# Optimization experiments

Measured on AMD Instinct MI355X. Metric: run time of the kernel, lower is better.

Reference implementation:

```python
import jax, jax.numpy as jnp
import numpy as np

NEG_BIG = -9e15
ALPHA = 0.2  # LeakyReLU negative slope


def setup_inputs() -> dict:
    key = jax.random.key(0)
    k1, k2, k3, k4 = jax.random.split(key, 4)
    B, N, Fin, Fout = 4, 2048, 128, 128
    h = jax.random.normal(k1, (B, N, Fin), dtype=jnp.float32)
    adj = jax.random.randint(k2, (N, N), 0, 2, dtype=jnp.int32)
    W = jax.random.normal(k3, (Fin, Fout), dtype=jnp.float32) * 0.1
    a = jax.random.normal(k4, (2 * Fout, 1), dtype=jnp.float32) * 0.1
    return {"h": h, "adj": adj, "W": W, "a": a}


def reference(h, adj, W, a):
    # Wh: [B, N, Fout]
    Wh = jnp.einsum('bnf,fo->bno', h, W)
    Fout = W.shape[1]
    a1 = a[:Fout, 0]   # attends to source i
    a2 = a[Fout:, 0]   # attends to target j
    # Decomposed form of leakyrelu(cat([Wh_i, Wh_j]) @ a):
    # e_ij = leakyrelu(a1.Wh_i + a2.Wh_j)  -> [B, N, N]
    f1 = Wh @ a1  # [B, N]
    f2 = Wh @ a2  # [B, N]
    e = jax.nn.leaky_relu(f1[:, :, None] + f2[:, None, :], negative_slope=ALPHA)
    attention = jnp.where(adj[None, :, :] > 0, e, jnp.float32(NEG_BIG))
    attention = jax.nn.softmax(attention, axis=2)
    # dropout is identity in eval mode
    h_prime = jnp.einsum('bij,bjo->bio', attention, Wh)
    return h_prime
```

## Files before the change

### kernel.cpp

```cpp
#include <hip/hip_runtime.h>

#define BB 4
#define NN 2048
#define FF 128
#define NP 2176
#define ALPHA 0.2f
#define SHIFT_C 16.0f

typedef short bf16x8 __attribute__((ext_vector_type(8)));
typedef float f32x4 __attribute__((ext_vector_type(4)));
typedef unsigned u32;

__device__ inline short f2bf(float f) {
    union { float f; unsigned u; } v; v.f = f;
    unsigned r = (v.u + 0x7FFFu + ((v.u >> 16) & 1u)) >> 16;
    return (short)r;
}
__device__ inline float bf2f(short s) {
    union { float f; unsigned u; } v;
    v.u = ((unsigned)(unsigned short)s) << 16;
    return v.f;
}

__global__ __launch_bounds__(256) void k_wh(const float* __restrict__ h,
                                            const float* __restrict__ W,
                                            const float* __restrict__ a,
                                            const int* __restrict__ adj,
                                            short* __restrict__ WhHiT,
                                            short* __restrict__ WhLoT,
                                            float* __restrict__ f1,
                                            float* __restrict__ f2,
                                            u32* __restrict__ adjp) {
    __shared__ float Wa[2 * FF];
    __shared__ float hs[16 * 128];
    int tid = threadIdx.x;
    int r0 = blockIdx.x * 16;

    {
        int fin = tid & 127;
        const float* av = (tid < 128) ? a : (a + FF);
        const float* wr = W + (size_t)fin * FF;
        float s = 0.f;
        for (int o = 0; o < FF; o += 4) {
            float4 wv = *(const float4*)(wr + o);
            float4 avv = *(const float4*)(av + o);
            s += wv.x * avv.x + wv.y * avv.y + wv.z * avv.z + wv.w * avv.w;
        }
        Wa[(tid < 128 ? 0 : FF) + fin] = s;
    }
    {
        const float4* src = (const float4*)(h + (size_t)r0 * FF);
        float4* dst = (float4*)hs;
        dst[tid] = src[tid];
        dst[256 + tid] = src[256 + tid];
    }
    {
        int g = blockIdx.x * 256 + tid;
        int row = g >> 6, wd = g & 63;
        const int4* ar = (const int4*)(adj + (size_t)row * NN + wd * 32);
        u32 word = 0;
#pragma unroll
        for (int q = 0; q < 8; ++q) {
            int4 v = ar[q];
            word |= (u32)(v.x > 0) << (q * 4);
            word |= (u32)(v.y > 0) << (q * 4 + 1);
            word |= (u32)(v.z > 0) << (q * 4 + 2);
            word |= (u32)(v.w > 0) << (q * 4 + 3);
        }
        adjp[row * 64 + wd] = word;
    }
    __syncthreads();

    {
        int w = tid >> 6, lane = tid & 63;
        float wa1_0 = Wa[lane], wa1_1 = Wa[lane + 64];
        float wa2_0 = Wa[FF + lane], wa2_1 = Wa[FF + lane + 64];
        for (int rr = 0; rr < 4; ++rr) {
            int rloc = w * 4 + rr;
            int row = r0 + rloc;
            float x0 = hs[rloc * FF + lane], x1 = hs[rloc * FF + lane + 64];
            float s1 = x0 * wa1_0 + x1 * wa1_1;
            float s2 = x0 * wa2_0 + x1 * wa2_1;
#pragma unroll
            for (int m = 32; m >= 1; m >>= 1) {
                s1 += __shfl_xor(s1, m, 64);
                s2 += __shfl_xor(s2, m, 64);
            }
            if (lane == 0) { f1[row] = s1; f2[row] = s2; }
        }
    }

    int f4 = (tid & 31) * 4;
    int rg = tid >> 5;
    float acc[2][4];
#pragma unroll
    for (int rr = 0; rr < 2; ++rr)
#pragma unroll
        for (int cc = 0; cc < 4; ++cc) acc[rr][cc] = 0.f;

    for (int k0 = 0; k0 < FF; k0 += 4) {
        float4 wv[4];
#pragma unroll
        for (int kk = 0; kk < 4; ++kk)
            wv[kk] = *(const float4*)(W + (size_t)(k0 + kk) * FF + f4);
        float4 hv[2];
#pragma unroll
        for (int rr = 0; rr < 2; ++rr)
            hv[rr] = *(const float4*)(hs + (rg * 2 + rr) * FF + k0);
#pragma unroll
        for (int rr = 0; rr < 2; ++rr) {
            float hk[4] = {hv[rr].x, hv[rr].y, hv[rr].z, hv[rr].w};
#pragma unroll
            for (int kk = 0; kk < 4; ++kk) {
                acc[rr][0] += hk[kk] * wv[kk].x;
                acc[rr][1] += hk[kk] * wv[kk].y;
                acc[rr][2] += hk[kk] * wv[kk].z;
                acc[rr][3] += hk[kk] * wv[kk].w;
            }
        }
    }
    int rloc = r0 + rg * 2;
    int b = rloc >> 11;
    int j = rloc & (NN - 1);
#pragma unroll
    for (int cc = 0; cc < 4; ++cc) {
        float v0 = acc[0][cc], v1 = acc[1][cc];
        short h0 = f2bf(v0), h1 = f2bf(v1);
        short l0 = f2bf(v0 - bf2f(h0)), l1 = f2bf(v1 - bf2f(h1));
        size_t off = (size_t)(b * FF + f4 + cc) * NP + j;
        *(short2*)(WhHiT + off) = make_short2(h0, h1);
        *(short2*)(WhLoT + off) = make_short2(l0, l1);
    }
}

#define EV(f2v, f1v, wv, bi) ({ float _t = (f1v) + (f2v); float _x = fmaxf(_t, ALPHA * _t); \
    __expf(_x - SHIFT_C) * (float)(((wv) >> (bi)) & 1u); })

__global__ __launch_bounds__(512) __attribute__((amdgpu_waves_per_eu(4, 4)))
void k_attn(const short* __restrict__ WhHiT,
            const short* __restrict__ WhLoT,
            const u32* __restrict__ adjp,
            const float* __restrict__ f1,
            const float* __restrict__ f2,
            float* __restrict__ out) {
    __shared__ __align__(16) char lds[66688];
    float* row_ps = (float*)(lds + 65536);
    float* row_inv = (float*)(lds + 66560);

    int tid = threadIdx.x;
    int w = tid >> 6, lane = tid & 63;
    int blk = blockIdx.x;
    int b = blk >> 7;
    int tile = (blk >> 1) & 63;
    int half = blk & 1;
    int i0 = tile * 32;

    int r_c = lane & 15, kg = lane >> 4;

    const float* f2b = f2 + b * NN;
    float f10 = f1[b * NN + i0 + r_c];
    float f11 = f1[b * NN + i0 + 16 + r_c];
    const u32* ap0 = adjp + (size_t)(i0 + r_c) * 64;
    const u32* ap1 = adjp + (size_t)(i0 + 16 + r_c) * 64;

    const ptrdiff_t dLo = (ptrdiff_t)BB * FF * NP;
    int s0 = w * 8;
    const short* pB0 = WhHiT + (size_t)(b * FF + half * 64 + 0 * 16 + r_c) * NP + s0 * 32 + kg * 8;
    const short* pB1 = WhHiT + (size_t)(b * FF + half * 64 + 1 * 16 + r_c) * NP + s0 * 32 + kg * 8;
    const short* pB2 = WhHiT + (size_t)(b * FF + half * 64 + 2 * 16 + r_c) * NP + s0 * 32 + kg * 8;
    const short* pB3 = WhHiT + (size_t)(b * FF + half * 64 + 3 * 16 + r_c) * NP + s0 * 32 + kg * 8;

    f32x4 acc0_0 = {0,0,0,0}, acc0_1 = {0,0,0,0};
    f32x4 acc1_0 = {0,0,0,0}, acc1_1 = {0,0,0,0};
    f32x4 acc2_0 = {0,0,0,0}, acc2_1 = {0,0,0,0};
    f32x4 acc3_0 = {0,0,0,0}, acc3_1 = {0,0,0,0};
    float sp0 = 0.f, sp1 = 0.f;

#pragma unroll 1
    for (int s8 = 0; s8 < 8; ++s8) {
        int s = s0 + s8;
        float4 q0 = *(const float4*)(f2b + s * 32 + kg * 8);
        float4 q1 = *(const float4*)(f2b + s * 32 + kg * 8 + 4);
        u32 w0 = ap0[s], w1 = ap1[s];
        bf16x8 bh0 = *(const bf16x8*)(pB0); bf16x8 bl0 = *(const bf16x8*)(pB0 + dLo);
        bf16x8 bh1 = *(const bf16x8*)(pB1); bf16x8 bl1 = *(const bf16x8*)(pB1 + dLo);
        bf16x8 bh2 = *(const bf16x8*)(pB2); bf16x8 bl2 = *(const bf16x8*)(pB2 + dLo);
        bf16x8 bh3 = *(const bf16x8*)(pB3); bf16x8 bl3 = *(const bf16x8*)(pB3 + dLo);

        union { u32 u[4]; bf16x8 v; } A0, A1;
        int bb = kg * 8;
        {
            float pa, pb;
            pa = EV(q0.x, f10, w0, bb + 0); pb = EV(q0.y, f10, w0, bb + 1);
            sp0 += pa + pb;
            asm("v_cvt_pk_bf16_f32 %0, %1, %2" : "=v"(A0.u[0]) : "v"(pa), "v"(pb));
            pa = EV(q0.z, f10, w0, bb + 2); pb = EV(q0.w, f10, w0, bb + 3);
            sp0 += pa + pb;
            asm("v_cvt_pk_bf16_f32 %0, %1, %2" : "=v"(A0.u[1]) : "v"(pa), "v"(pb));
            pa = EV(q1.x, f10, w0, bb + 4); pb = EV(q1.y, f10, w0, bb + 5);
            sp0 += pa + pb;
            asm("v_cvt_pk_bf16_f32 %0, %1, %2" : "=v"(A0.u[2]) : "v"(pa), "v"(pb));
            pa = EV(q1.z, f10, w0, bb + 6); pb = EV(q1.w, f10, w0, bb + 7);
            sp0 += pa + pb;
            asm("v_cvt_pk_bf16_f32 %0, %1, %2" : "=v"(A0.u[3]) : "v"(pa), "v"(pb));

            pa = EV(q0.x, f11, w1, bb + 0); pb = EV(q0.y, f11, w1, bb + 1);
            sp1 += pa + pb;
            asm("v_cvt_pk_bf16_f32 %0, %1, %2" : "=v"(A1.u[0]) : "v"(pa), "v"(pb));
            pa = EV(q0.z, f11, w1, bb + 2); pb = EV(q0.w, f11, w1, bb + 3);
            sp1 += pa + pb;
            asm("v_cvt_pk_bf16_f32 %0, %1, %2" : "=v"(A1.u[1]) : "v"(pa), "v"(pb));
            pa = EV(q1.x, f11, w1, bb + 4); pb = EV(q1.y, f11, w1, bb + 5);
            sp1 += pa + pb;
            asm("v_cvt_pk_bf16_f32 %0, %1, %2" : "=v"(A1.u[2]) : "v"(pa), "v"(pb));
            pa = EV(q1.z, f11, w1, bb + 6); pb = EV(q1.w, f11, w1, bb + 7);
            sp1 += pa + pb;
            asm("v_cvt_pk_bf16_f32 %0, %1, %2" : "=v"(A1.u[3]) : "v"(pa), "v"(pb));
        }

        acc0_0 = __builtin_amdgcn_mfma_f32_16x16x32_bf16(A0.v, bh0, acc0_0, 0, 0, 0);
        acc0_0 = __builtin_amdgcn_mfma_f32_16x16x32_bf16(A0.v, bl0, acc0_0, 0, 0, 0);
        acc0_1 = __builtin_amdgcn_mfma_f32_16x16x32_bf16(A1.v, bh0, acc0_1, 0, 0, 0);
        acc0_1 = __builtin_amdgcn_mfma_f32_16x16x32_bf16(A1.v, bl0, acc0_1, 0, 0, 0);
        acc1_0 = __builtin_amdgcn_mfma_f32_16x16x32_bf16(A0.v, bh1, acc1_0, 0, 0, 0);
        acc1_0 = __builtin_amdgcn_mfma_f32_16x16x32_bf16(A0.v, bl1, acc1_0, 0, 0, 0);
        acc1_1 = __builtin_amdgcn_mfma_f32_16x16x32_bf16(A1.v, bh1, acc1_1, 0, 0, 0);
        acc1_1 = __builtin_amdgcn_mfma_f32_16x16x32_bf16(A1.v, bl1, acc1_1, 0, 0, 0);
        acc2_0 = __builtin_amdgcn_mfma_f32_16x16x32_bf16(A0.v, bh2, acc2_0, 0, 0, 0);
        acc2_0 = __builtin_amdgcn_mfma_f32_16x16x32_bf16(A0.v, bl2, acc2_0, 0, 0, 0);
        acc2_1 = __builtin_amdgcn_mfma_f32_16x16x32_bf16(A1.v, bh2, acc2_1, 0, 0, 0);
        acc2_1 = __builtin_amdgcn_mfma_f32_16x16x32_bf16(A1.v, bl2, acc2_1, 0, 0, 0);
        acc3_0 = __builtin_amdgcn_mfma_f32_16x16x32_bf16(A0.v, bh3, acc3_0, 0, 0, 0);
        acc3_0 = __builtin_amdgcn_mfma_f32_16x16x32_bf16(A0.v, bl3, acc3_0, 0, 0, 0);
        acc3_1 = __builtin_amdgcn_mfma_f32_16x16x32_bf16(A1.v, bh3, acc3_1, 0, 0, 0);
        acc3_1 = __builtin_amdgcn_mfma_f32_16x16x32_bf16(A1.v, bl3, acc3_1, 0, 0, 0);

        pB0 += 32; pB1 += 32; pB2 += 32; pB3 += 32;
    }

    sp0 += __shfl_xor(sp0, 16, 64); sp0 += __shfl_xor(sp0, 32, 64);
    sp1 += __shfl_xor(sp1, 16, 64); sp1 += __shfl_xor(sp1, 32, 64);
    if (lane < 16) {
        row_ps[w * 32 + lane] = sp0;
        row_ps[w * 32 + 16 + lane] = sp1;
    }
    {
        char* img = lds + w * 8192;
#define STACC(NI, MI, A) { int ch = (((NI)*16 + r_c) * 8 + (MI)*4 + kg) ^ (r_c & 7); \
                           *(f32x4*)(img + ch * 16) = (A); }
        STACC(0, 0, acc0_0) STACC(0, 1, acc0_1)
        STACC(1, 0, acc1_0) STACC(1, 1, acc1_1)
        STACC(2, 0, acc2_0) STACC(2, 1, acc2_1)
        STACC(3, 0, acc3_0) STACC(3, 1, acc3_1)
#undef STACC
    }
    __syncthreads();
    if (tid < 32) {
        float t = 0.f;
#pragma unroll
        for (int ww = 0; ww < 8; ++ww) t += row_ps[ww * 32 + tid];
        row_inv[tid] = 1.0f / t;
    }
    __syncthreads();

    {
        int colg = w * 8 + (lane >> 3);
        int rq = lane & 7;
        int ch = (colg * 8 + rq) ^ (colg & 7);
        f32x4 v = {0, 0, 0, 0};
#pragma unroll
        for (int im = 0; im < 8; ++im)
            v += *(const f32x4*)(lds + im * 8192 + ch * 16);
        f32x4 rinv = *(const f32x4*)((char*)row_inv + rq * 16);
        float* ob = out + ((size_t)b * NN + i0 + rq * 4) * FF + half * 64 + colg;
#pragma unroll
        for (int q = 0; q < 4; ++q)
            ob[(size_t)q * FF] = v[q] * rinv[q];
    }
}

extern "C" void kernel_launch(void* const* d_in, const int* in_sizes, int n_in,
                              void* d_out, int out_size, void* d_ws, size_t ws_size,
                              hipStream_t stream) {
    const float* h   = (const float*)d_in[0];
    const int*   adj = (const int*)d_in[1];
    const float* W   = (const float*)d_in[2];
    const float* a   = (const float*)d_in[3];
    float* out = (float*)d_out;

    short* WhHiT = (short*)d_ws;
    short* WhLoT = WhHiT + (size_t)BB * FF * NP;
    float* f1 = (float*)(WhLoT + (size_t)BB * FF * NP);
    float* f2 = f1 + (size_t)BB * NN;
    u32* adjp = (u32*)(f2 + (size_t)BB * NN);

    k_wh<<<(BB * NN) / 16, 256, 0, stream>>>(h, W, a, adj, WhHiT, WhLoT, f1, f2, adjp);
    k_attn<<<512, 512, 0, stream>>>(WhHiT, WhLoT, adjp, f1, f2, out);
}
```

Before: 133.2 us.

## Split attention output columns into quarters to double grid and shrink LDS

Each k_attn block now computes 32 output features instead of 64, so the grid grows from 512 to 1024 blocks and per-thread accumulators halve. The cross-wave reduction uses half the LDS: waves 0-3 store partials, waves 4-7 add theirs in place, and the final pass sums 4 images instead of 8. This is meant to raise occupancy and parallelism on the 256-CU part. In exchange, the exp/softmax score computation and the f2/adjacency loads are duplicated across four blocks instead of two.

Result: slower. 241.5 us (+81.3%).

```diff
diff --git a/kernel.cpp b/kernel.cpp
--- a/kernel.cpp
+++ b/kernel.cpp
@@ -136,23 +136,23 @@
 #define EV(f2v, f1v, wv, bi) ({ float _t = (f1v) + (f2v); float _x = fmaxf(_t, ALPHA * _t); \
     __expf(_x - SHIFT_C) * (float)(((wv) >> (bi)) & 1u); })
 
-__global__ __launch_bounds__(512) __attribute__((amdgpu_waves_per_eu(4, 4)))
+__global__ __launch_bounds__(512, 8)
 void k_attn(const short* __restrict__ WhHiT,
             const short* __restrict__ WhLoT,
             const u32* __restrict__ adjp,
             const float* __restrict__ f1,
             const float* __restrict__ f2,
             float* __restrict__ out) {
-    __shared__ __align__(16) char lds[66688];
-    float* row_ps = (float*)(lds + 65536);
-    float* row_inv = (float*)(lds + 66560);
+    __shared__ __align__(16) char lds[17536];
+    float* row_ps = (float*)(lds + 16384);
+    float* row_inv = (float*)(lds + 17408);
 
     int tid = threadIdx.x;
     int w = tid >> 6, lane = tid & 63;
     int blk = blockIdx.x;
-    int b = blk >> 7;
-    int tile = (blk >> 1) & 63;
-    int half = blk & 1;
+    int b = blk >> 8;
+    int tile = (blk >> 2) & 63;
+    int qt = blk & 3;
     int i0 = tile * 32;
 
     int r_c = lane & 15, kg = lane >> 4;
@@ -165,15 +165,11 @@
 
     const ptrdiff_t dLo = (ptrdiff_t)BB * FF * NP;
     int s0 = w * 8;
-    const short* pB0 = WhHiT + (size_t)(b * FF + half * 64 + 0 * 16 + r_c) * NP + s0 * 32 + kg * 8;
-    const short* pB1 = WhHiT + (size_t)(b * FF + half * 64 + 1 * 16 + r_c) * NP + s0 * 32 + kg * 8;
-    const short* pB2 = WhHiT + (size_t)(b * FF + half * 64 + 2 * 16 + r_c) * NP + s0 * 32 + kg * 8;
-    const short* pB3 = WhHiT + (size_t)(b * FF + half * 64 + 3 * 16 + r_c) * NP + s0 * 32 + kg * 8;
+    const short* pB0 = WhHiT + (size_t)(b * FF + qt * 32 + 0 * 16 + r_c) * NP + s0 * 32 + kg * 8;
+    const short* pB1 = WhHiT + (size_t)(b * FF + qt * 32 + 1 * 16 + r_c) * NP + s0 * 32 + kg * 8;
 
     f32x4 acc0_0 = {0,0,0,0}, acc0_1 = {0,0,0,0};
     f32x4 acc1_0 = {0,0,0,0}, acc1_1 = {0,0,0,0};
-    f32x4 acc2_0 = {0,0,0,0}, acc2_1 = {0,0,0,0};
-    f32x4 acc3_0 = {0,0,0,0}, acc3_1 = {0,0,0,0};
     float sp0 = 0.f, sp1 = 0.f;
 
 #pragma unroll 1
@@ -184,8 +180,6 @@
         u32 w0 = ap0[s], w1 = ap1[s];
         bf16x8 bh0 = *(const bf16x8*)(pB0); bf16x8 bl0 = *(const bf16x8*)(pB0 + dLo);
         bf16x8 bh1 = *(const bf16x8*)(pB1); bf16x8 bl1 = *(const bf16x8*)(pB1 + dLo);
-        bf16x8 bh2 = *(const bf16x8*)(pB2); bf16x8 bl2 = *(const bf16x8*)(pB2 + dLo);
-        bf16x8 bh3 = *(const bf16x8*)(pB3); bf16x8 bl3 = *(const bf16x8*)(pB3 + dLo);
 
         union { u32 u[4]; bf16x8 v; } A0, A1;
         int bb = kg * 8;
@@ -226,16 +220,8 @@
         acc1_0 = __builtin_amdgcn_mfma_f32_16x16x32_bf16(A0.v, bl1, acc1_0, 0, 0, 0);
         acc1_1 = __builtin_amdgcn_mfma_f32_16x16x32_bf16(A1.v, bh1, acc1_1, 0, 0, 0);
         acc1_1 = __builtin_amdgcn_mfma_f32_16x16x32_bf16(A1.v, bl1, acc1_1, 0, 0, 0);
-        acc2_0 = __builtin_amdgcn_mfma_f32_16x16x32_bf16(A0.v, bh2, acc2_0, 0, 0, 0);
-        acc2_0 = __builtin_amdgcn_mfma_f32_16x16x32_bf16(A0.v, bl2, acc2_0, 0, 0, 0);
-        acc2_1 = __builtin_amdgcn_mfma_f32_16x16x32_bf16(A1.v, bh2, acc2_1, 0, 0, 0);
-        acc2_1 = __builtin_amdgcn_mfma_f32_16x16x32_bf16(A1.v, bl2, acc2_1, 0, 0, 0);
-        acc3_0 = __builtin_amdgcn_mfma_f32_16x16x32_bf16(A0.v, bh3, acc3_0, 0, 0, 0);
-        acc3_0 = __builtin_amdgcn_mfma_f32_16x16x32_bf16(A0.v, bl3, acc3_0, 0, 0, 0);
-        acc3_1 = __builtin_amdgcn_mfma_f32_16x16x32_bf16(A1.v, bh3, acc3_1, 0, 0, 0);
-        acc3_1 = __builtin_amdgcn_mfma_f32_16x16x32_bf16(A1.v, bl3, acc3_1, 0, 0, 0);
-
-        pB0 += 32; pB1 += 32; pB2 += 32; pB3 += 32;
+
+        pB0 += 32; pB1 += 32;
     }
 
     sp0 += __shfl_xor(sp0, 16, 64); sp0 += __shfl_xor(sp0, 32, 64);
@@ -244,18 +230,23 @@
         row_ps[w * 32 + lane] = sp0;
         row_ps[w * 32 + 16 + lane] = sp1;
     }
-    {
-        char* img = lds + w * 8192;
+    if (w < 4) {
+        char* img = lds + w * 4096;
 #define STACC(NI, MI, A) { int ch = (((NI)*16 + r_c) * 8 + (MI)*4 + kg) ^ (r_c & 7); \
                            *(f32x4*)(img + ch * 16) = (A); }
         STACC(0, 0, acc0_0) STACC(0, 1, acc0_1)
         STACC(1, 0, acc1_0) STACC(1, 1, acc1_1)
-        STACC(2, 0, acc2_0) STACC(2, 1, acc2_1)
-        STACC(3, 0, acc3_0) STACC(3, 1, acc3_1)
 #undef STACC
     }
     __syncthreads();
-    if (tid < 32) {
+    if (w >= 4) {
+        char* img = lds + (w - 4) * 4096;
+#define MRGACC(NI, MI, A) { int ch = (((NI)*16 + r_c) * 8 + (MI)*4 + kg) ^ (r_c & 7); \
+                            f32x4* p = (f32x4*)(img + ch * 16); *p = *p + (A); }
+        MRGACC(0, 0, acc0_0) MRGACC(0, 1, acc0_1)
+        MRGACC(1, 0, acc1_0) MRGACC(1, 1, acc1_1)
+#undef MRGACC
+    } else if (tid < 32) {
         float t = 0.f;
 #pragma unroll
         for (int ww = 0; ww < 8; ++ww) t += row_ps[ww * 32 + tid];
@@ -263,16 +254,16 @@
     }
     __syncthreads();
 
-    {
-        int colg = w * 8 + (lane >> 3);
+    if (lane < 32) {
+        int colg = w * 4 + (lane >> 3);
         int rq = lane & 7;
         int ch = (colg * 8 + rq) ^ (colg & 7);
         f32x4 v = {0, 0, 0, 0};
 #pragma unroll
-        for (int im = 0; im < 8; ++im)
-            v += *(const f32x4*)(lds + im * 8192 + ch * 16);
+        for (int im = 0; im < 4; ++im)
+            v += *(const f32x4*)(lds + im * 4096 + ch * 16);
         f32x4 rinv = *(const f32x4*)((char*)row_inv + rq * 16);
-        float* ob = out + ((size_t)b * NN + i0 + rq * 4) * FF + half * 64 + colg;
+        float* ob = out + ((size_t)b * NN + i0 + rq * 4) * FF + qt * 32 + colg;
 #pragma unroll
         for (int q = 0; q < 4; ++q)
             ob[(size_t)q * FF] = v[q] * rinv[q];
@@ -295,5 +286,5 @@
     u32* adjp = (u32*)(f2 + (size_t)BB * NN);
 
     k_wh<<<(BB * NN) / 16, 256, 0, stream>>>(h, W, a, adj, WhHiT, WhLoT, f1, f2, adjp);
-    k_attn<<<512, 512, 0, stream>>>(WhHiT, WhLoT, adjp, f1, f2, out);
-}
+    k_attn<<<1024, 512, 0, stream>>>(WhHiT, WhLoT, adjp, f1, f2, out);
+}
```
